# Optimization experiments

Measured on AMD Instinct MI355X. Metric: run time of the kernel, lower is better.

The kernel has to match this reference:

```python
import jax, jax.numpy as jnp
import numpy as np

H = 2048        # hidden_size
NH = 32         # num_heads
HD = H // NH    # head_dim = 64
S = 512         # seq_len
UP = 2          # upsample_ratio
SU = S * UP     # upsampled seq len = 1024
INTER = 5632    # GatedMLP intermediate: int(2048*4*2/3) rounded up to mult of 256
EPS = 1e-6
DEPTH = 1


def rmsnorm(x, w):
    var = jnp.mean(jnp.square(x), axis=-1, keepdims=True)
    return x * jax.lax.rsqrt(var + EPS) * w


def setup_inputs() -> dict:
    key = jax.random.key(0)
    ks = jax.random.split(key, 12)
    sc = 0.02
    return {
        "hidden_states": jax.random.normal(ks[0], (2, S, H), dtype=jnp.float32),
        "W_up": jax.random.normal(ks[1], (SU, S), dtype=jnp.float32) * sc,
        "b_up": jnp.zeros((SU,), dtype=jnp.float32),
        "attn_norm_w": jnp.ones((H,), dtype=jnp.float32),
        "Wq": jax.random.normal(ks[2], (H, H), dtype=jnp.float32) * sc,
        "Wk": jax.random.normal(ks[3], (H, H), dtype=jnp.float32) * sc,
        "Wv": jax.random.normal(ks[4], (H, H), dtype=jnp.float32) * sc,
        "Wo": jax.random.normal(ks[5], (H, H), dtype=jnp.float32) * sc,
        "mlp_norm_w": jnp.ones((H,), dtype=jnp.float32),
        "Wg": jax.random.normal(ks[6], (INTER, H), dtype=jnp.float32) * sc,
        "Wu": jax.random.normal(ks[7], (INTER, H), dtype=jnp.float32) * sc,
        "Wd": jax.random.normal(ks[8], (H, INTER), dtype=jnp.float32) * sc,
    }


def reference(hidden_states, W_up, b_up, attn_norm_w, Wq, Wk, Wv, Wo,
              mlp_norm_w, Wg, Wu, Wd):
    B = hidden_states.shape[0]
    # init_upsampled_tokens: Linear over the sequence axis
    # up[b,t,d] = sum_s h[b,s,d] * W_up[t,s] + b_up[t]
    up = jnp.einsum('bsd,ts->btd', hidden_states, W_up) + b_up[None, :, None]

    for _ in range(DEPTH):
        residual = jnp.concatenate([hidden_states, up], axis=-2)  # [B, S+SU, H]
        x = rmsnorm(up, attn_norm_w)                               # [B, SU, H]
        q = (x @ Wq.T).reshape(B, SU, NH, HD)
        k = (residual @ Wk.T).reshape(B, S + SU, NH, HD)
        v = (residual @ Wv.T).reshape(B, S + SU, NH, HD)
        # explicit (non-causal) cross-attention, full score matrix
        scores = jnp.einsum('bshd,bthd->bsht', q, k) / np.sqrt(HD).astype(np.float32)
        attn = jax.nn.softmax(scores, axis=-1)
        o = jnp.einsum('bsht,bthd->bshd', attn, v).reshape(B, SU, H)
        x = (o @ Wo.T) + x                 # residual onto the *normed* tokens
        x = rmsnorm(x, mlp_norm_w)
        mlp_out = (jax.nn.silu(x @ Wg.T) * (x @ Wu.T)) @ Wd.T
        up = mlp_out + x
    return up
```

## Files before the change

### kernel.cpp

```cpp
#include <hip/hip_runtime.h>

typedef __bf16 bf16;
typedef __bf16 bf16x8 __attribute__((ext_vector_type(8)));
typedef float  f32x4  __attribute__((ext_vector_type(4)));
typedef unsigned int u32x4 __attribute__((ext_vector_type(4)));

#define NB 2
#define SS 512
#define HH 2048
#define SUx 1024
#define TT 1536
#define INTERx 5632

__device__ __forceinline__ void gload16(const void* g, void* l)
{
    __builtin_amdgcn_global_load_lds(
        (const __attribute__((address_space(1))) void*)g,
        (__attribute__((address_space(3))) void*)l, 16, 0, 0);
}

struct CastArgs {
    const float* src[10];
    bf16*        dst[10];
    int          blk0[11];
};

__global__ __launch_bounds__(256)
void cast_all_k(CastArgs a)
{
    int b = blockIdx.x;
    int s = 0;
    #pragma unroll
    for (int i = 1; i < 10; ++i) if (b >= a.blk0[i]) s = i;
    long idx = ((long)(b - a.blk0[s]) * 256 + threadIdx.x) * 8;
    const float* in = a.src[s];
    bf16* out = a.dst[s];
    f32x4 va = *(const f32x4*)(in + idx);
    f32x4 vb = *(const f32x4*)(in + idx + 4);
    bf16x8 o;
    o[0]=(bf16)va[0]; o[1]=(bf16)va[1]; o[2]=(bf16)va[2]; o[3]=(bf16)va[3];
    o[4]=(bf16)vb[0]; o[5]=(bf16)vb[1]; o[6]=(bf16)vb[2]; o[7]=(bf16)vb[3];
    *(bf16x8*)(out + idx) = o;
}

template <typename TIN>
__global__ __launch_bounds__(256)
void transpose_k(const TIN* __restrict__ in, bf16* __restrict__ out,
                 int inRS, int outRS, int nz2,
                 long inZ1, long inZ2, long outZ1, long outZ2)
{
    __shared__ bf16 tile[64][65];
    int z1 = blockIdx.z / nz2, z2 = blockIdx.z % nz2;
    const TIN* ip = in + (long)z1*inZ1 + (long)z2*inZ2
                  + (long)blockIdx.x*64*inRS + (long)blockIdx.y*64;
    bf16* op = out + (long)z1*outZ1 + (long)z2*outZ2
             + (long)blockIdx.y*64*outRS + (long)blockIdx.x*64;
    int tc = threadIdx.x & 63, tr = threadIdx.x >> 6;
    #pragma unroll
    for (int rr = 0; rr < 64; rr += 4)
        tile[rr+tr][tc] = (bf16)(float)ip[(long)(rr+tr)*inRS + tc];
    __syncthreads();
    #pragma unroll
    for (int cc = 0; cc < 64; cc += 4)
        op[(long)(cc+tr)*outRS + tc] = tile[tc][cc+tr];
}

__global__ __launch_bounds__(256)
void rmsnorm_k(const float* __restrict__ x, const float* __restrict__ w,
               bf16* __restrict__ yb, float* __restrict__ yf)
{
    long row = blockIdx.x;
    const float* xp = x + row * HH;
    int t = threadIdx.x;
    f32x4 v0 = *(const f32x4*)(xp + t*8);
    f32x4 v1 = *(const f32x4*)(xp + t*8 + 4);
    float ss = 0.f;
    #pragma unroll
    for (int j = 0; j < 4; ++j) ss += v0[j]*v0[j] + v1[j]*v1[j];
    #pragma unroll
    for (int off = 32; off > 0; off >>= 1) ss += __shfl_xor(ss, off);
    __shared__ float red[4];
    if ((t & 63) == 0) red[t >> 6] = ss;
    __syncthreads();
    float tot = red[0] + red[1] + red[2] + red[3];
    float inv = rsqrtf(tot * (1.0f/(float)HH) + 1e-6f);
    f32x4 w0 = *(const f32x4*)(w + t*8);
    f32x4 w1 = *(const f32x4*)(w + t*8 + 4);
    f32x4 y0, y1; bf16x8 ob;
    #pragma unroll
    for (int j = 0; j < 4; ++j) {
        y0[j] = v0[j] * inv * w0[j];
        y1[j] = v1[j] * inv * w1[j];
        ob[j]   = (bf16)y0[j];
        ob[4+j] = (bf16)y1[j];
    }
    *(bf16x8*)(yb + row*HH + t*8) = ob;
    if (yf) {
        *(f32x4*)(yf + row*HH + t*8)     = y0;
        *(f32x4*)(yf + row*HH + t*8 + 4) = y1;
    }
}

template <int GU>
__device__ __forceinline__
void gemm_body(const bf16* __restrict__ A, const bf16* __restrict__ Bw,
               int Nsplit, int K,
               long sA, long sB,
               bf16* __restrict__ Cb, bf16* __restrict__ Cb2, long sCb,
               float* __restrict__ C32, long sC32,
               const float* __restrict__ res, long sRes,
               const float* __restrict__ bias,
               float scale, int doSilu,
               int lin, int gx, int nwg,
               bf16* Asmem, bf16* Bsmem)
{
    int z = blockIdx.z;
    const bf16* Ap = A + (long)z * sA;

    int qq = nwg >> 3, r8 = nwg & 7;
    int xcd = lin & 7, off = lin >> 3;
    int wg = (xcd < r8 ? xcd * (qq + 1) : r8 * (qq + 1) + (xcd - r8) * qq) + off;
    int n0 = (wg % gx) * 128, m0 = (wg / gx) * 128;

    int t = threadIdx.x, lane = t & 63, w = t >> 6;
    int wr = w >> 2, wc = w & 3;
    int lc = lane & 15, lg = lane >> 4;

    int lr = lane >> 3, ls = lane & 7;
    const bf16* gA[2]; const bf16* gB[2];
    int ldsOff[2];
    #pragma unroll
    for (int i = 0; i < 2; ++i) {
        int r = (i*8 + w)*8 + lr;
        gA[i] = Ap + (long)(m0 + r) * K + (ls ^ lr) * 8;
        if (GU) {
            long grow = (long)(n0 >> 1) + (r >> 1);
            gB[i] = Bw + ((r & 1) ? (long)INTERx * K : 0) + grow * K + (ls ^ lr) * 8;
        } else {
            const bf16* Bp = Bw + (long)z * sB;
            gB[i] = Bp + (long)(n0 + r) * K + (ls ^ lr) * 8;
        }
        ldsOff[i] = (i*8 + w) * 512;
    }

    f32x4 zero = {0.f, 0.f, 0.f, 0.f};
    f32x4 acc[4][2];
    #pragma unroll
    for (int i = 0; i < 4; ++i)
        #pragma unroll
        for (int j = 0; j < 2; ++j) acc[i][j] = zero;

    int NKI = K >> 6;
    #pragma unroll
    for (int i = 0; i < 2; ++i) {
        gload16(gA[i], Asmem + ldsOff[i]);
        gload16(gB[i], Bsmem + ldsOff[i]);
    }
    if (NKI > 1) {
        #pragma unroll
        for (int i = 0; i < 2; ++i) {
            gload16(gA[i] + 64, Asmem + 128*64 + ldsOff[i]);
            gload16(gB[i] + 64, Bsmem + 128*64 + ldsOff[i]);
        }
    }

    for (int ks = 0; ks < NKI; ++ks) {
        int cur = ks & 1;
        const bf16* Asc = Asmem + cur * (128*64);
        const bf16* Bsc = Bsmem + cur * (128*64);

        if (ks == NKI - 1) asm volatile("s_waitcnt vmcnt(0)" ::: "memory");
        else               asm volatile("s_waitcnt vmcnt(4)" ::: "memory");
        __builtin_amdgcn_s_barrier();
        __builtin_amdgcn_sched_barrier(0);

        #pragma unroll
        for (int kk = 0; kk < 2; ++kk) {
            bf16x8 af[4], bfv[2];
            #pragma unroll
            for (int i = 0; i < 4; ++i) {
                int rA = wr*64 + i*16 + lc;
                af[i]  = *(const bf16x8*)(Asc + rA*64 + (((kk*4 + lg) ^ (rA & 7)) * 8));
            }
            #pragma unroll
            for (int j = 0; j < 2; ++j) {
                int rB = wc*32 + j*16 + lc;
                bfv[j] = *(const bf16x8*)(Bsc + rB*64 + (((kk*4 + lg) ^ (rB & 7)) * 8));
            }
            __builtin_amdgcn_s_setprio(1);
            #pragma unroll
            for (int i = 0; i < 4; ++i)
                #pragma unroll
                for (int j = 0; j < 2; ++j)
                    acc[i][j] = __builtin_amdgcn_mfma_f32_16x16x32_bf16(af[i], bfv[j], acc[i][j], 0, 0, 0);
            __builtin_amdgcn_s_setprio(0);
        }

        __builtin_amdgcn_s_barrier();
        if (ks + 2 < NKI) {
            long ko = (long)(ks + 2) * 64;
            #pragma unroll
            for (int i = 0; i < 2; ++i) {
                gload16(gA[i] + ko, (bf16*)Asc + ldsOff[i]);
                gload16(gB[i] + ko, (bf16*)Bsc + ldsOff[i]);
            }
        }
    }

    if (GU) {
        #pragma unroll
        for (int i = 0; i < 4; ++i) {
            #pragma unroll
            for (int j = 0; j < 2; ++j) {
                int tc2 = wc*32 + j*16 + lc;
                int colp = (n0 >> 1) + (tc2 >> 1);
                #pragma unroll
                for (int r = 0; r < 4; ++r) {
                    int row = m0 + wr*64 + i*16 + lg*4 + r;
                    float v = acc[i][j][r];
                    float pv = __shfl_xor(v, 1);
                    float g  = (lc & 1) ? pv : v;
                    float uu = (lc & 1) ? v  : pv;
                    float prod = (g / (1.f + __expf(-g))) * uu;
                    if (!(lc & 1))
                        Cb[(long)row * Nsplit + colp] = (bf16)prod;
                }
            }
        }
    } else {
        #pragma unroll
        for (int i = 0; i < 4; ++i) {
            #pragma unroll
            for (int j = 0; j < 2; ++j) {
                int col = n0 + wc*32 + j*16 + lc;
                bf16* dst = Cb; int c2 = col;
                if (Cb2 && col >= Nsplit) { dst = Cb2; c2 = col - Nsplit; }
                int firstHalf = (col < Nsplit);
                #pragma unroll
                for (int r = 0; r < 4; ++r) {
                    int row = m0 + wr*64 + i*16 + lg*4 + r;
                    float v = acc[i][j][r] * scale;
                    if (bias)   v += bias[row];
                    if (doSilu && firstHalf) v = v / (1.f + __expf(-v));
                    long off = (long)row * Nsplit + c2;
                    if (res)  v += res[(long)z * sRes + off];
                    if (C32)  C32[(long)z * sC32 + off] = v;
                    if (dst)  dst[(long)z * sCb + off] = (bf16)v;
                }
            }
        }
    }
}

template <int GU>
__global__ __launch_bounds__(512)
void gemm_k(const bf16* __restrict__ A, const bf16* __restrict__ Bw,
            int Nsplit, int K,
            long sA, long sB,
            bf16* __restrict__ Cb, bf16* __restrict__ Cb2, long sCb,
            float* __restrict__ C32, long sC32,
            const float* __restrict__ res, long sRes,
            const float* __restrict__ bias,
            float scale, int doSilu)
{
    __shared__ alignas(16) bf16 As[2][128 * 64];
    __shared__ alignas(16) bf16 Bs[2][128 * 64];
    int gx = gridDim.x;
    int nwg = gx * gridDim.y;
    int lin = blockIdx.y * gx + blockIdx.x;
    gemm_body<GU>(A, Bw, Nsplit, K, sA, sB, Cb, Cb2, sCb, C32, sC32,
                  res, sRes, bias, scale, doSilu, lin, gx, nwg,
                  &As[0][0], &Bs[0][0]);
}

__global__ __launch_bounds__(512)
void qkv_k(const bf16* __restrict__ x1b, const bf16* __restrict__ wq,
           bf16* __restrict__ qb,
           const bf16* __restrict__ resb, const bf16* __restrict__ wk,
           bf16* __restrict__ kb, bf16* __restrict__ vb)
{
    __shared__ alignas(16) bf16 As[2][128 * 64];
    __shared__ alignas(16) bf16 Bs[2][128 * 64];
    int lin = blockIdx.x;
    if (lin < 256) {
        gemm_body<0>(x1b, wq, HH, HH, 0, 0, qb, nullptr, 0, nullptr, 0,
                     nullptr, 0, nullptr, 0.125f, 0, lin, 16, 256,
                     &As[0][0], &Bs[0][0]);
    } else {
        gemm_body<0>(resb, wk, HH, HH, 0, 0, kb, vb, 0, nullptr, 0,
                     nullptr, 0, nullptr, 1.0f, 0, lin - 256, 32, 768,
                     &As[0][0], &Bs[0][0]);
    }
}

__global__ __launch_bounds__(512)
void attn_k(const bf16* __restrict__ q, const bf16* __restrict__ k,
            const bf16* __restrict__ vt, bf16* __restrict__ o)
{
    int qc = blockIdx.x, h = blockIdx.y, b = blockIdx.z;
    int t = threadIdx.x, lane = t & 63, w = t >> 6;
    int lc = lane & 15, lg = lane >> 4;
    const bf16* qp = q  + ((long)(b*SUx + qc*256 + w*32)) * HH + h*64;
    const bf16* kp = k  + ((long)b*TT) * HH + h*64;
    const bf16* vp = vt + ((long)(b*32 + h)) * 64 * TT;

    __shared__ alignas(16) bf16 Ks[2][64*64];
    __shared__ alignas(16) bf16 Vs[2][64*64];
    __shared__ alignas(16) bf16 Ps[8][2][16*72];

    bf16x8 qf[2][2];
    #pragma unroll
    for (int s = 0; s < 2; ++s)
        #pragma unroll
        for (int kk = 0; kk < 2; ++kk)
            qf[s][kk] = *(const bf16x8*)(qp + (long)(s*16 + lc)*HH + kk*32 + lg*8);

    int lr = lane >> 3, ls = lane & 7;
    int srow = w*8 + lr;
    int sslot = ls ^ lr;
    const bf16* gK = kp + (long)srow * HH + sslot*8;
    const bf16* gV = vp + (long)srow * TT + sslot*8;
    int ldsO = w * 512;

    f32x4 zero = {0.f, 0.f, 0.f, 0.f};
    f32x4 oacc[2][4];
    float lsum[2][4];
    #pragma unroll
    for (int qs = 0; qs < 2; ++qs) {
        #pragma unroll
        for (int r = 0; r < 4; ++r) lsum[qs][r] = 0.f;
        #pragma unroll
        for (int dt = 0; dt < 4; ++dt) oacc[qs][dt] = zero;
    }

    const int NS = TT / 64;
    gload16(gK,            &Ks[0][0] + ldsO);
    gload16(gV,            &Vs[0][0] + ldsO);
    gload16(gK + 64L*HH,   &Ks[1][0] + ldsO);
    gload16(gV + 64,       &Vs[1][0] + ldsO);

    for (int st = 0; st < NS; ++st) {
        int cur = st & 1;
        const bf16* Kc = &Ks[cur][0];
        const bf16* Vc = &Vs[cur][0];

        if (st == NS - 1) asm volatile("s_waitcnt vmcnt(0)" ::: "memory");
        else              asm volatile("s_waitcnt vmcnt(2)" ::: "memory");
        __builtin_amdgcn_s_barrier();
        __builtin_amdgcn_sched_barrier(0);

        bf16x8 kf[4][2];
        #pragma unroll
        for (int s2 = 0; s2 < 4; ++s2) {
            int row = s2*16 + lc;
            #pragma unroll
            for (int kk = 0; kk < 2; ++kk)
                kf[s2][kk] = *(const bf16x8*)(Kc + row*64 + (((kk*4 + lg) ^ (row & 7)) * 8));
        }
        f32x4 sv[2][4];
        __builtin_amdgcn_s_setprio(1);
        #pragma unroll
        for (int qs = 0; qs < 2; ++qs)
            #pragma unroll
            for (int s2 = 0; s2 < 4; ++s2) {
                f32x4 a0 = __builtin_amdgcn_mfma_f32_16x16x32_bf16(qf[qs][0], kf[s2][0], zero, 0, 0, 0);
                sv[qs][s2] = __builtin_amdgcn_mfma_f32_16x16x32_bf16(qf[qs][1], kf[s2][1], a0, 0, 0, 0);
            }
        __builtin_amdgcn_s_setprio(0);

        bf16* Pw = &Ps[w][0][0];
        #pragma unroll
        for (int qs = 0; qs < 2; ++qs)
            #pragma unroll
            for (int r = 0; r < 4; ++r) {
                int prow = lg*4 + r;
                #pragma unroll
                for (int s2 = 0; s2 < 4; ++s2) {
                    float pp = __expf(sv[qs][s2][r]);
                    lsum[qs][r] += pp;
                    Pw[qs*(16*72) + prow*72 + s2*16 + lc] = (bf16)pp;
                }
            }
        asm volatile("s_waitcnt lgkmcnt(0)" ::: "memory");
        __builtin_amdgcn_sched_barrier(0);

        bf16x8 pf[2][2];
        #pragma unroll
        for (int qs = 0; qs < 2; ++qs)
            #pragma unroll
            for (int ks = 0; ks < 2; ++ks)
                pf[qs][ks] = *(const bf16x8*)(Pw + qs*(16*72) + lc*72 + (ks*4 + lg)*8);
        bf16x8 vf[4][2];
        #pragma unroll
        for (int dt = 0; dt < 4; ++dt) {
            int row = dt*16 + lc;
            #pragma unroll
            for (int ks = 0; ks < 2; ++ks)
                vf[dt][ks] = *(const bf16x8*)(Vc + row*64 + (((ks*4 + lg) ^ (row & 7)) * 8));
        }
        __builtin_amdgcn_s_setprio(1);
        #pragma unroll
        for (int qs = 0; qs < 2; ++qs)
            #pragma unroll
            for (int dt = 0; dt < 4; ++dt) {
                oacc[qs][dt] = __builtin_amdgcn_mfma_f32_16x16x32_bf16(pf[qs][0], vf[dt][0], oacc[qs][dt], 0, 0, 0);
                oacc[qs][dt] = __builtin_amdgcn_mfma_f32_16x16x32_bf16(pf[qs][1], vf[dt][1], oacc[qs][dt], 0, 0, 0);
            }
        __builtin_amdgcn_s_setprio(0);

        __builtin_amdgcn_s_barrier();
        if (st + 2 < NS) {
            long t2 = (long)(st + 2) * 64;
            gload16(gK + t2*HH, (bf16*)Kc + ldsO);
            gload16(gV + t2,    (bf16*)Vc + ldsO);
        }
    }

    #pragma unroll
    for (int qs = 0; qs < 2; ++qs)
        #pragma unroll
        for (int r = 0; r < 4; ++r) {
            float l = lsum[qs][r];
            l += __shfl_xor(l, 1);
            l += __shfl_xor(l, 2);
            l += __shfl_xor(l, 4);
            l += __shfl_xor(l, 8);
            float inv = 1.0f / l;
            long row = (long)b*SUx + qc*256 + w*32 + qs*16 + lg*4 + r;
            #pragma unroll
            for (int dt = 0; dt < 4; ++dt)
                o[row*HH + h*64 + dt*16 + lc] = (bf16)(oacc[qs][dt][r] * inv);
        }
}

extern "C" void kernel_launch(void* const* d_in, const int* in_sizes, int n_in,
                              void* d_out, int out_size, void* d_ws, size_t ws_size,
                              hipStream_t stream)
{
    const float* hs  = (const float*)d_in[0];
    const float* Wup = (const float*)d_in[1];
    const float* bup = (const float*)d_in[2];
    const float* anw = (const float*)d_in[3];
    const float* Wq  = (const float*)d_in[4];
    const float* Wk  = (const float*)d_in[5];
    const float* Wv  = (const float*)d_in[6];
    const float* Wo  = (const float*)d_in[7];
    const float* mnw = (const float*)d_in[8];
    const float* Wg  = (const float*)d_in[9];
    const float* Wu  = (const float*)d_in[10];
    const float* Wd  = (const float*)d_in[11];
    float* outp = (float*)d_out;

    char* p = (char*)d_ws;
    auto take = [&](size_t bytes) -> void* {
        void* r = (void*)p;
        p += (bytes + 255) & ~(size_t)255;
        return r;
    };

    bf16* wq  = (bf16*)take((size_t)HH*HH*2);
    bf16* wk  = (bf16*)take(2 * (size_t)HH*HH*2);
    bf16* wv  = wk + (size_t)HH*HH;
    bf16* wo  = (bf16*)take((size_t)HH*HH*2);
    bf16* wgu = (bf16*)take(2 * (size_t)INTERx*HH*2);
    bf16* wd  = (bf16*)take((size_t)INTERx*HH*2);
    bf16* wup = (bf16*)take((size_t)SUx*SS*2);
    bf16* ht  = (bf16*)take((size_t)NB*HH*SS*2);
    bf16* resb= (bf16*)take((size_t)NB*TT*HH*2);
    float* x1f= (float*)take((size_t)NB*SUx*HH*4);
    bf16* x1b = (bf16*)take((size_t)NB*SUx*HH*2);
    float* upf= (float*)take((size_t)NB*SUx*HH*4);

    size_t attn_bytes = (size_t)NB*SUx*HH*2 + 3*(size_t)NB*TT*HH*2 + (size_t)NB*SUx*HH*2;
    size_t mlp_bytes  = (size_t)NB*SUx*HH*4 + (size_t)NB*SUx*HH*2 + (size_t)NB*SUx*INTERx*2;
    char* un = (char*)take(attn_bytes > mlp_bytes ? attn_bytes : mlp_bytes);
    bf16* qb  = (bf16*)un;
    bf16* kb  = qb  + (size_t)NB*SUx*HH;
    bf16* vb  = kb  + (size_t)NB*TT*HH;
    bf16* vtb = vb  + (size_t)NB*TT*HH;
    bf16* ob  = vtb + (size_t)NB*TT*HH;
    float* x2f= (float*)un;
    bf16* x2b = (bf16*)(un + (size_t)NB*SUx*HH*4);
    bf16* gb  = x2b + (size_t)NB*SUx*HH;

    CastArgs ca;
    int blk = 0;
    auto seg = [&](int i, const float* s, bf16* d, long nelem) {
        ca.src[i] = s; ca.dst[i] = d; ca.blk0[i] = blk;
        blk += (int)(nelem / 2048);
    };
    seg(0, Wq,  wq,  (long)HH*HH);
    seg(1, Wk,  wk,  (long)HH*HH);
    seg(2, Wv,  wv,  (long)HH*HH);
    seg(3, Wo,  wo,  (long)HH*HH);
    seg(4, Wg,  wgu, (long)INTERx*HH);
    seg(5, Wu,  wgu + (size_t)INTERx*HH, (long)INTERx*HH);
    seg(6, Wd,  wd,  (long)INTERx*HH);
    seg(7, Wup, wup, (long)SUx*SS);
    seg(8, hs,                 resb,                   (long)SS*HH);
    seg(9, hs + (size_t)SS*HH, resb + (size_t)TT*HH,   (long)SS*HH);
    ca.blk0[10] = blk;
    cast_all_k<<<dim3(blk), 256, 0, stream>>>(ca);

    transpose_k<float><<<dim3(SS/64, HH/64, NB), 256, 0, stream>>>(
        hs, ht, HH, SS, 1, (long)SS*HH, 0, (long)HH*SS, 0);

    gemm_k<0><<<dim3(HH/128, SUx/128, NB), 512, 0, stream>>>(
        wup, ht, HH, SS, 0, (long)HH*SS,
        resb + (size_t)SS*HH, nullptr, (long)TT*HH,
        upf, (long)SUx*HH,
        nullptr, 0, bup, 1.0f, 0);

    rmsnorm_k<<<dim3(NB*SUx), 256, 0, stream>>>(upf, anw, x1b, x1f);

    qkv_k<<<dim3(1024), 512, 0, stream>>>(x1b, wq, qb, resb, wk, kb, vb);

    transpose_k<bf16><<<dim3(TT/64, 1, NB*32), 256, 0, stream>>>(
        vb, vtb, HH, TT, 32, (long)TT*HH, 64, (long)32*64*TT, (long)64*TT);

    attn_k<<<dim3(SUx/256, 32, NB), 512, 0, stream>>>(qb, kb, vtb, ob);

    gemm_k<0><<<dim3(HH/128, (NB*SUx)/128, 1), 512, 0, stream>>>(
        ob, wo, HH, HH, 0, 0, nullptr, nullptr, 0, upf, 0, x1f, 0, nullptr, 1.0f, 0);

    rmsnorm_k<<<dim3(NB*SUx), 256, 0, stream>>>(upf, mnw, x2b, x2f);

    gemm_k<1><<<dim3((2*INTERx)/128, (NB*SUx)/128, 1), 512, 0, stream>>>(
        x2b, wgu, INTERx, HH, 0, 0, gb, nullptr, 0, nullptr, 0, nullptr, 0, nullptr, 1.0f, 0);

    gemm_k<0><<<dim3(HH/128, (NB*SUx)/128, 1), 512, 0, stream>>>(
        gb, wd, HH, INTERx, 0, 0, nullptr, nullptr, 0, outp, 0, x2f, 0, nullptr, 1.0f, 0);

    (void)in_sizes; (void)n_in; (void)out_size; (void)ws_size;
}
```

Baseline: 482.0 us.

## Use 4-wave GEMM workgroups with 64x64 per-wave tiles

Changes the shared 128x128 GEMM body from 8 waves, each computing a 64x32 sub-tile, to 4 waves, each computing a 64x64 sub-tile. Each thread now issues four async global-to-LDS loads per operand per K-step, and the waitcnt threshold and launch sizes are updated to match. The aim is more MFMA work per LDS fragment load, raising arithmetic intensity per wave and cutting barrier and coordination overhead. In exchange it doubles accumulator registers per thread and halves the waves available to hide latency.

New measurement: 525.1 us. +8.9%, slower.

```diff
diff --git a/kernel.cpp b/kernel.cpp
--- a/kernel.cpp
+++ b/kernel.cpp
@@ -123,46 +123,46 @@
     int n0 = (wg % gx) * 128, m0 = (wg / gx) * 128;
 
     int t = threadIdx.x, lane = t & 63, w = t >> 6;
-    int wr = w >> 2, wc = w & 3;
+    int wr = w >> 1, wc = w & 1;
     int lc = lane & 15, lg = lane >> 4;
 
-    int lr = lane >> 3, ls = lane & 7;
-    const bf16* gA[2]; const bf16* gB[2];
-    int ldsOff[2];
-    #pragma unroll
-    for (int i = 0; i < 2; ++i) {
-        int r = (i*8 + w)*8 + lr;
-        gA[i] = Ap + (long)(m0 + r) * K + (ls ^ lr) * 8;
+    int sr = t >> 3, ss_ = t & 7;
+    const bf16* gA[4]; const bf16* gB[4];
+    int ldsO[4];
+    #pragma unroll
+    for (int i = 0; i < 4; ++i) {
+        int r = i*32 + sr;
+        gA[i] = Ap + (long)(m0 + r) * K + ((ss_ ^ (r & 7)) * 8);
         if (GU) {
             long grow = (long)(n0 >> 1) + (r >> 1);
-            gB[i] = Bw + ((r & 1) ? (long)INTERx * K : 0) + grow * K + (ls ^ lr) * 8;
+            gB[i] = Bw + ((r & 1) ? (long)INTERx * K : 0) + grow * K + ((ss_ ^ (r & 7)) * 8);
         } else {
             const bf16* Bp = Bw + (long)z * sB;
-            gB[i] = Bp + (long)(n0 + r) * K + (ls ^ lr) * 8;
-        }
-        ldsOff[i] = (i*8 + w) * 512;
+            gB[i] = Bp + (long)(n0 + r) * K + ((ss_ ^ (r & 7)) * 8);
+        }
+        ldsO[i] = i * 2048 + t * 8;
     }
 
     f32x4 zero = {0.f, 0.f, 0.f, 0.f};
-    f32x4 acc[4][2];
+    f32x4 acc[4][4];
     #pragma unroll
     for (int i = 0; i < 4; ++i)
         #pragma unroll
-        for (int j = 0; j < 2; ++j) acc[i][j] = zero;
+        for (int j = 0; j < 4; ++j) acc[i][j] = zero;
+
+    auto stage = [&](int buf, int ti) {
+        long ko = (long)ti * 64;
+        #pragma unroll
+        for (int i = 0; i < 4; ++i)
+            gload16(gA[i] + ko, Asmem + buf*(128*64) + ldsO[i]);
+        #pragma unroll
+        for (int i = 0; i < 4; ++i)
+            gload16(gB[i] + ko, Bsmem + buf*(128*64) + ldsO[i]);
+    };
 
     int NKI = K >> 6;
-    #pragma unroll
-    for (int i = 0; i < 2; ++i) {
-        gload16(gA[i], Asmem + ldsOff[i]);
-        gload16(gB[i], Bsmem + ldsOff[i]);
-    }
-    if (NKI > 1) {
-        #pragma unroll
-        for (int i = 0; i < 2; ++i) {
-            gload16(gA[i] + 64, Asmem + 128*64 + ldsOff[i]);
-            gload16(gB[i] + 64, Bsmem + 128*64 + ldsOff[i]);
-        }
-    }
+    stage(0, 0);
+    if (NKI > 1) stage(1, 1);
 
     for (int ks = 0; ks < NKI; ++ks) {
         int cur = ks & 1;
@@ -170,49 +170,42 @@
         const bf16* Bsc = Bsmem + cur * (128*64);
 
         if (ks == NKI - 1) asm volatile("s_waitcnt vmcnt(0)" ::: "memory");
-        else               asm volatile("s_waitcnt vmcnt(4)" ::: "memory");
+        else               asm volatile("s_waitcnt vmcnt(8)" ::: "memory");
         __builtin_amdgcn_s_barrier();
         __builtin_amdgcn_sched_barrier(0);
 
         #pragma unroll
         for (int kk = 0; kk < 2; ++kk) {
-            bf16x8 af[4], bfv[2];
+            bf16x8 af[4], bfv[4];
             #pragma unroll
             for (int i = 0; i < 4; ++i) {
                 int rA = wr*64 + i*16 + lc;
                 af[i]  = *(const bf16x8*)(Asc + rA*64 + (((kk*4 + lg) ^ (rA & 7)) * 8));
             }
             #pragma unroll
-            for (int j = 0; j < 2; ++j) {
-                int rB = wc*32 + j*16 + lc;
+            for (int j = 0; j < 4; ++j) {
+                int rB = wc*64 + j*16 + lc;
                 bfv[j] = *(const bf16x8*)(Bsc + rB*64 + (((kk*4 + lg) ^ (rB & 7)) * 8));
             }
             __builtin_amdgcn_s_setprio(1);
             #pragma unroll
             for (int i = 0; i < 4; ++i)
                 #pragma unroll
-                for (int j = 0; j < 2; ++j)
+                for (int j = 0; j < 4; ++j)
                     acc[i][j] = __builtin_amdgcn_mfma_f32_16x16x32_bf16(af[i], bfv[j], acc[i][j], 0, 0, 0);
             __builtin_amdgcn_s_setprio(0);
         }
 
         __builtin_amdgcn_s_barrier();
-        if (ks + 2 < NKI) {
-            long ko = (long)(ks + 2) * 64;
-            #pragma unroll
-            for (int i = 0; i < 2; ++i) {
-                gload16(gA[i] + ko, (bf16*)Asc + ldsOff[i]);
-                gload16(gB[i] + ko, (bf16*)Bsc + ldsOff[i]);
-            }
-        }
+        if (ks + 2 < NKI) stage(cur, ks + 2);
     }
 
     if (GU) {
         #pragma unroll
         for (int i = 0; i < 4; ++i) {
             #pragma unroll
-            for (int j = 0; j < 2; ++j) {
-                int tc2 = wc*32 + j*16 + lc;
+            for (int j = 0; j < 4; ++j) {
+                int tc2 = wc*64 + j*16 + lc;
                 int colp = (n0 >> 1) + (tc2 >> 1);
                 #pragma unroll
                 for (int r = 0; r < 4; ++r) {
@@ -231,8 +224,8 @@
         #pragma unroll
         for (int i = 0; i < 4; ++i) {
             #pragma unroll
-            for (int j = 0; j < 2; ++j) {
-                int col = n0 + wc*32 + j*16 + lc;
+            for (int j = 0; j < 4; ++j) {
+                int col = n0 + wc*64 + j*16 + lc;
                 bf16* dst = Cb; int c2 = col;
                 if (Cb2 && col >= Nsplit) { dst = Cb2; c2 = col - Nsplit; }
                 int firstHalf = (col < Nsplit);
@@ -253,7 +246,7 @@
 }
 
 template <int GU>
-__global__ __launch_bounds__(512)
+__global__ __launch_bounds__(256)
 void gemm_k(const bf16* __restrict__ A, const bf16* __restrict__ Bw,
             int Nsplit, int K,
             long sA, long sB,
@@ -273,7 +266,7 @@
                   &As[0][0], &Bs[0][0]);
 }
 
-__global__ __launch_bounds__(512)
+__global__ __launch_bounds__(256)
 void qkv_k(const bf16* __restrict__ x1b, const bf16* __restrict__ wq,
            bf16* __restrict__ qb,
            const bf16* __restrict__ resb, const bf16* __restrict__ wk,
@@ -505,7 +498,7 @@
     transpose_k<float><<<dim3(SS/64, HH/64, NB), 256, 0, stream>>>(
         hs, ht, HH, SS, 1, (long)SS*HH, 0, (long)HH*SS, 0);
 
-    gemm_k<0><<<dim3(HH/128, SUx/128, NB), 512, 0, stream>>>(
+    gemm_k<0><<<dim3(HH/128, SUx/128, NB), 256, 0, stream>>>(
         wup, ht, HH, SS, 0, (long)HH*SS,
         resb + (size_t)SS*HH, nullptr, (long)TT*HH,
         upf, (long)SUx*HH,
@@ -513,22 +506,22 @@
 
     rmsnorm_k<<<dim3(NB*SUx), 256, 0, stream>>>(upf, anw, x1b, x1f);
 
-    qkv_k<<<dim3(1024), 512, 0, stream>>>(x1b, wq, qb, resb, wk, kb, vb);
+    qkv_k<<<dim3(1024), 256, 0, stream>>>(x1b, wq, qb, resb, wk, kb, vb);
 
     transpose_k<bf16><<<dim3(TT/64, 1, NB*32), 256, 0, stream>>>(
         vb, vtb, HH, TT, 32, (long)TT*HH, 64, (long)32*64*TT, (long)64*TT);
 
     attn_k<<<dim3(SUx/256, 32, NB), 512, 0, stream>>>(qb, kb, vtb, ob);
 
-    gemm_k<0><<<dim3(HH/128, (NB*SUx)/128, 1), 512, 0, stream>>>(
+    gemm_k<0><<<dim3(HH/128, (NB*SUx)/128, 1), 256, 0, stream>>>(
         ob, wo, HH, HH, 0, 0, nullptr, nullptr, 0, upf, 0, x1f, 0, nullptr, 1.0f, 0);
 
     rmsnorm_k<<<dim3(NB*SUx), 256, 0, stream>>>(upf, mnw, x2b, x2f);
 
-    gemm_k<1><<<dim3((2*INTERx)/128, (NB*SUx)/128, 1), 512, 0, stream>>>(
+    gemm_k<1><<<dim3((2*INTERx)/128, (NB*SUx)/128, 1), 256, 0, stream>>>(
         x2b, wgu, INTERx, HH, 0, 0, gb, nullptr, 0, nullptr, 0, nullptr, 0, nullptr, 1.0f, 0);
 
-    gemm_k<0><<<dim3(HH/128, (NB*SUx)/128, 1), 512, 0, stream>>>(
+    gemm_k<0><<<dim3(HH/128, (NB*SUx)/128, 1), 256, 0, stream>>>(
         gb, wd, HH, INTERx, 0, 0, nullptr, nullptr, 0, outp, 0, x2f, 0, nullptr, 1.0f, 0);
 
     (void)in_sizes; (void)n_in; (void)out_size; (void)ws_size;
```
